# Performance work log

Measured on AMD Instinct MI355X. Metric: run time of the kernel, lower is better.

Reference implementation:

```python
import jax, jax.numpy as jnp
import numpy as np

GRID = 7          # grid_unit
NSAMPLE = 48      # sample_num
RADIUS = 0.3      # radiu_grid
FEAT = 128


def square_distance(src, dst):
    # src [B,N,C], dst [B,M,C] -> [B,N,M]
    d = -2.0 * jnp.einsum('bnc,bmc->bnm', src, dst)
    d = d + jnp.sum(src * src, -1)[:, :, None]
    d = d + jnp.sum(dst * dst, -1)[:, None, :]
    return d


def batch_norm(x):
    n = jnp.sqrt(jnp.sum(x * x, axis=2, keepdims=True) + 1e-8)
    return x / (n + 1e-10)


def query_ball_point(radius, nsample, xyz, new_xyz):
    B, N, _ = xyz.shape
    sqr = square_distance(new_xyz, xyz)                       # [B,S,N]
    gidx = jnp.where(sqr > radius ** 2, N, jnp.arange(N)[None, None, :])
    gidx = jnp.sort(gidx, axis=-1)[:, :, :nsample]            # [B,S,ns]
    first = gidx[:, :, :1]
    return jnp.where(gidx == N, first, gidx)


def index_points(points, idx):
    # points [B,N,C], idx [B,S,K] -> [B,S,K,C]
    return jax.vmap(lambda p, i: p[i])(points, idx)


def _forward(xyz, pts_feat, W0, b0, W1, b1, W_unet, index):
    B = xyz.shape[0]
    pts = jnp.transpose(xyz[:, 0:3, :], (0, 2, 1))            # [B,N,3]
    N = pts.shape[1]
    g = GRID

    # mlp0 / mlp1 (Conv1d(128,3,1)) + batch_norm
    oris = batch_norm(pts_feat @ W0.T + b0)                   # [B,N,3]
    nors = batch_norm(pts_feat @ W1.T + b1)                   # [B,N,3]

    # ---- rot_pts_3D ----
    gidx = query_ball_point(RADIUS, NSAMPLE, pts, pts)        # [B,N,48]
    group_pts = index_points(pts, gidx)                       # [B,N,48,3]
    group_feat = index_points(pts_feat, gidx).reshape(-1, NSAMPLE, FEAT)  # [BN,48,128]

    ori_rot90 = batch_norm(jnp.cross(oris, nors))
    ori_0 = batch_norm(jnp.cross(ori_rot90, nors))
    rot = jnp.concatenate([ori_0, ori_rot90, nors], axis=-1).reshape(-1, 3, 3)
    rot = jnp.transpose(rot, (0, 2, 1))                       # [BN,3,3]

    local = (group_pts - pts[:, :, None, :]).reshape(-1, NSAMPLE, 3)
    local_pts = jnp.einsum('bsc,bcd->bsd', local, rot)        # [BN,48,3]

    coords = jnp.round((local_pts + RADIUS) / (2 * RADIUS) * (g - 1)).astype(jnp.int32)
    coords = jnp.clip(coords, 0, g - 1)
    # faithful to the original flattening: x*g + y*g + z
    idx = coords[..., 0] * g + coords[..., 1] * g + coords[..., 2]  # [BN,48]

    BN = local_pts.shape[0]
    grid0 = jnp.zeros((BN, g * g * g, FEAT), dtype=pts_feat.dtype)
    feat3d = grid0.at[jnp.arange(BN)[:, None], idx].set(group_feat)  # [BN,343,128]

    # ---- UNet3D stand-in: [BN,128,7,7,7] -> [BN,3,7,7] via (channel,depth) projection
    feat5d = feat3d.reshape(BN, g, g, g, FEAT)
    feat_off = jnp.einsum('bijkc,ckd->bijd', feat5d, W_unet).reshape(BN, g * g, 3)

    # ---- rot_offset ----
    vals = jnp.array([[i * 0.01, j * 0.01, 0.0]
                      for i in range(-30, 36, 10)
                      for j in range(-30, 36, 10)], dtype=pts.dtype)   # [49,3]
    up = vals[None] + feat_off                                # [BN,49,3]
    pts_repeat = pts.reshape(-1, 1, 3)                        # [BN,1,3]
    pts_up = jnp.einsum('bsc,bdc->bsd', up, rot) + pts_repeat  # v @ rot^T

    pts_offset = pts_up[:, 24, :].reshape(B, -1, 3)           # [B,N,3]
    pts_ups = pts_up[:, index, :].reshape(B, -1, 3)           # [B,16N,3]
    return (oris, nors, pts_ups, pts_offset, pts_up)


def setup_inputs() -> dict:
    key = jax.random.key(0)
    ks = jax.random.split(key, 6)
    B, N, C = 2, 1024, 128
    xyz = jax.random.normal(ks[0], (B, 3, N), dtype=jnp.float32)
    pts_feat = jax.random.normal(ks[1], (B, N, C), dtype=jnp.float32)
    W0 = jax.random.normal(ks[2], (3, C), dtype=jnp.float32) * 0.05
    b0 = jnp.zeros((3,), dtype=jnp.float32)
    W1 = jax.random.normal(ks[3], (3, C), dtype=jnp.float32) * 0.05
    b1 = jnp.zeros((3,), dtype=jnp.float32)
    W_unet = jax.random.normal(ks[4], (C, GRID, 3), dtype=jnp.float32) * 0.02
    index = jax.random.randint(ks[5], (16,), 0, GRID * GRID)
    return {"xyz": xyz, "pts_feat": pts_feat, "W0": W0, "b0": b0,
            "W1": W1, "b1": b1, "W_unet": W_unet, "index": index}


def reference(xyz, pts_feat, W0, b0, W1, b1, W_unet, index):
    return _forward(xyz, pts_feat, W0, b0, W1, b1, W_unet, index)
```

## Files before the change

kernel.cpp:

```cpp
#include <hip/hip_runtime.h>

#define NB 2
#define NP 1024
#define NC 128
#define NG 7
#define NSM 48
#define BN (NB*NP)

#define OFF_ORIS 0
#define OFF_NORS (BN*3)
#define OFF_PUPS (2*BN*3)
#define OFF_POFF (OFF_PUPS + BN*16*3)
#define OFF_PU   (OFF_POFF + BN*3)

__device__ __forceinline__ void bnorm3(float v[3]) {
    float ss = __fadd_rn(__fadd_rn(__fmul_rn(v[0],v[0]), __fmul_rn(v[1],v[1])), __fmul_rn(v[2],v[2]));
    float nr = sqrtf(__fadd_rn(ss, 1e-8f));
    float dn = __fadd_rn(nr, 1e-10f);
    v[0] = __fdiv_rn(v[0], dn);
    v[1] = __fdiv_rn(v[1], dn);
    v[2] = __fdiv_rn(v[2], dn);
}

__global__ __launch_bounds__(64) void k1(const float* __restrict__ xyz,
                                         const float* __restrict__ feat,
                                         const float* __restrict__ W0, const float* __restrict__ b0,
                                         const float* __restrict__ W1, const float* __restrict__ b1,
                                         float* __restrict__ out,
                                         float* __restrict__ pts_ws,
                                         float* __restrict__ nrm_ws,
                                         float* __restrict__ rot_ws) {
    int p = blockIdx.x;
    int b = p >> 10, n = p & (NP - 1);
    int l = threadIdx.x;

    float f0 = feat[p*NC + l];
    float f1 = feat[p*NC + 64 + l];
    float s0 = f0*W0[l]     + f1*W0[64+l];
    float s1 = f0*W0[128+l] + f1*W0[192+l];
    float s2 = f0*W0[256+l] + f1*W0[320+l];
    float s3 = f0*W1[l]     + f1*W1[64+l];
    float s4 = f0*W1[128+l] + f1*W1[192+l];
    float s5 = f0*W1[256+l] + f1*W1[320+l];
    for (int off = 32; off; off >>= 1) {
        s0 += __shfl_xor(s0, off);
        s1 += __shfl_xor(s1, off);
        s2 += __shfl_xor(s2, off);
        s3 += __shfl_xor(s3, off);
        s4 += __shfl_xor(s4, off);
        s5 += __shfl_xor(s5, off);
    }
    if (l == 0) {
        float o[3]  = { s0 + b0[0], s1 + b0[1], s2 + b0[2] };
        float nn[3] = { s3 + b1[0], s4 + b1[1], s5 + b1[2] };
        bnorm3(o);
        bnorm3(nn);
        float r90[3];
        r90[0] = __fsub_rn(__fmul_rn(o[1], nn[2]), __fmul_rn(o[2], nn[1]));
        r90[1] = __fsub_rn(__fmul_rn(o[2], nn[0]), __fmul_rn(o[0], nn[2]));
        r90[2] = __fsub_rn(__fmul_rn(o[0], nn[1]), __fmul_rn(o[1], nn[0]));
        bnorm3(r90);
        float o0[3];
        o0[0] = __fsub_rn(__fmul_rn(r90[1], nn[2]), __fmul_rn(r90[2], nn[1]));
        o0[1] = __fsub_rn(__fmul_rn(r90[2], nn[0]), __fmul_rn(r90[0], nn[2]));
        o0[2] = __fsub_rn(__fmul_rn(r90[0], nn[1]), __fmul_rn(r90[1], nn[0]));
        bnorm3(o0);

        out[OFF_ORIS + p*3+0] = o[0];  out[OFF_ORIS + p*3+1] = o[1];  out[OFF_ORIS + p*3+2] = o[2];
        out[OFF_NORS + p*3+0] = nn[0]; out[OFF_NORS + p*3+1] = nn[1]; out[OFF_NORS + p*3+2] = nn[2];

        rot_ws[p*9+0] = o0[0];  rot_ws[p*9+1] = o0[1];  rot_ws[p*9+2] = o0[2];
        rot_ws[p*9+3] = r90[0]; rot_ws[p*9+4] = r90[1]; rot_ws[p*9+5] = r90[2];
        rot_ws[p*9+6] = nn[0];  rot_ws[p*9+7] = nn[1];  rot_ws[p*9+8] = nn[2];

        float px = xyz[(b*3+0)*NP + n];
        float py = xyz[(b*3+1)*NP + n];
        float pz = xyz[(b*3+2)*NP + n];
        pts_ws[p*3+0] = px; pts_ws[p*3+1] = py; pts_ws[p*3+2] = pz;
        nrm_ws[p] = __fadd_rn(__fadd_rn(__fmul_rn(px,px), __fmul_rn(py,py)), __fmul_rn(pz,pz));
    }
}

__global__ __launch_bounds__(256) void k2(const float* __restrict__ feat,
                                          const float* __restrict__ W_unet,
                                          const int* __restrict__ index,
                                          const float* __restrict__ pts_ws,
                                          const float* __restrict__ nrm_ws,
                                          const float* __restrict__ rot_ws,
                                          float* __restrict__ out) {
    __shared__ float spts[NP*3];
    __shared__ float snrm[NP];
    __shared__ float srot[9];
    __shared__ int   sgidx[NSM];
    __shared__ int   sidx[NSM];
    __shared__ int   swin[NSM];
    __shared__ float sfo[NG*NG*3];
    __shared__ float spu[NG*NG*3];

    int p = blockIdx.x;
    int b = p >> 10, n = p & (NP - 1);
    int tid = threadIdx.x;

    for (int i = tid; i < NP*3; i += 256) spts[i] = pts_ws[b*NP*3 + i];
    for (int i = tid; i < NP; i += 256)   snrm[i] = nrm_ws[b*NP + i];
    if (tid < 9) srot[tid] = rot_ws[p*9 + tid];
    if (tid < NG*NG*3) sfo[tid] = 0.0f;
    __syncthreads();

    if (tid < 64) {
        float cx = spts[n*3+0], cy = spts[n*3+1], cz = spts[n*3+2];
        float cn = snrm[n];
        int count = 0, first = -1;
        for (int base = 0; base < NP && count < NSM; base += 64) {
            int m = base + tid;
            float dot = __fadd_rn(__fadd_rn(__fmul_rn(cx, spts[m*3+0]),
                                            __fmul_rn(cy, spts[m*3+1])),
                                  __fmul_rn(cz, spts[m*3+2]));
            float d = __fadd_rn(__fadd_rn(__fmul_rn(-2.0f, dot), cn), snrm[m]);
            bool sel = !(d > 0.09f);
            unsigned long long mk = __ballot(sel);
            if (first < 0 && mk != 0ull) first = base + (__ffsll(mk) - 1);
            if (sel) {
                int pos = count + (int)__popcll(mk & ((1ull << tid) - 1ull));
                if (pos < NSM) sgidx[pos] = m;
            }
            count += (int)__popcll(mk);
        }
        if (first < 0) first = n;
        if (count < NSM) {
            for (int i = count + tid; i < NSM; i += 64) sgidx[i] = first;
        }
    }
    __syncthreads();

    if (tid < NSM) {
        int m = sgidx[tid];
        float lx = spts[m*3+0] - spts[n*3+0];
        float ly = spts[m*3+1] - spts[n*3+1];
        float lz = spts[m*3+2] - spts[n*3+2];
        int c[3];
        #pragma unroll
        for (int dd = 0; dd < 3; ++dd) {
            float lp = __fadd_rn(__fadd_rn(__fmul_rn(lx, srot[dd*3+0]),
                                           __fmul_rn(ly, srot[dd*3+1])),
                                 __fmul_rn(lz, srot[dd*3+2]));
            float t = rintf(__fmul_rn(__fdiv_rn(__fadd_rn(lp, 0.3f), 0.6f), 6.0f));
            int ci = (int)t;
            ci = ci < 0 ? 0 : (ci > 6 ? 6 : ci);
            c[dd] = ci;
        }
        sidx[tid] = c[0]*NG + c[1]*NG + c[2];
    }
    __syncthreads();

    if (tid < NSM) {
        int w = 1, my = sidx[tid];
        for (int s2 = tid + 1; s2 < NSM; ++s2)
            if (sidx[s2] == my) { w = 0; break; }
        swin[tid] = w;
    }
    __syncthreads();

    {
        int wid = tid >> 6, lane = tid & 63;
        for (int s = wid; s < NSM; s += 4) {
            if (!swin[s]) continue;
            int cell = sidx[s];
            int k = cell % NG;
            int q = cell / NG;
            int m = sgidx[s];
            const float* fr = feat + (size_t)(b*NP + m) * NC;
            float p0 = 0.f, p1 = 0.f, p2 = 0.f;
            #pragma unroll
            for (int cc = lane; cc < NC; cc += 64) {
                float f = fr[cc];
                const float* w = W_unet + cc*(NG*3) + k*3;
                p0 += f * w[0];
                p1 += f * w[1];
                p2 += f * w[2];
            }
            for (int off = 32; off; off >>= 1) {
                p0 += __shfl_xor(p0, off);
                p1 += __shfl_xor(p1, off);
                p2 += __shfl_xor(p2, off);
            }
            if (lane == 0) {
                atomicAdd(&sfo[q*3+0], p0);
                atomicAdd(&sfo[q*3+1], p1);
                atomicAdd(&sfo[q*3+2], p2);
            }
        }
    }
    __syncthreads();

    if (tid < NG*NG*3) {
        int q = tid / 3, d = tid % 3;
        int qi = q / NG, qj = q % NG;
        float v0 = (float)((-30 + 10*qi) * 0.01);
        float v1 = (float)((-30 + 10*qj) * 0.01);
        float u0 = __fadd_rn(v0, sfo[q*3+0]);
        float u1 = __fadd_rn(v1, sfo[q*3+1]);
        float u2 = sfo[q*3+2];
        float r = __fadd_rn(
                    __fadd_rn(
                      __fadd_rn(__fmul_rn(u0, srot[0*3+d]), __fmul_rn(u1, srot[1*3+d])),
                      __fmul_rn(u2, srot[2*3+d])),
                    spts[n*3+d]);
        spu[tid] = r;
        out[OFF_PU + p*(NG*NG*3) + tid] = r;
        if (q == 24) out[OFF_POFF + p*3 + d] = r;
    }
    __syncthreads();

    if (tid < 16*3) {
        int t = tid / 3, d = tid % 3;
        int q = index[t];
        out[OFF_PUPS + (p*16 + t)*3 + d] = spu[q*3 + d];
    }
}

extern "C" void kernel_launch(void* const* d_in, const int* in_sizes, int n_in,
                              void* d_out, int out_size, void* d_ws, size_t ws_size,
                              hipStream_t stream) {
    const float* xyz    = (const float*)d_in[0];
    const float* feat   = (const float*)d_in[1];
    const float* W0     = (const float*)d_in[2];
    const float* b0     = (const float*)d_in[3];
    const float* W1     = (const float*)d_in[4];
    const float* b1     = (const float*)d_in[5];
    const float* W_unet = (const float*)d_in[6];
    const int*   index  = (const int*)d_in[7];
    float* out = (float*)d_out;
    float* ws  = (float*)d_ws;

    float* pts_ws = ws;
    float* nrm_ws = ws + BN*3;
    float* rot_ws = ws + BN*3 + BN;

    hipLaunchKernelGGL(k1, dim3(BN), dim3(64), 0, stream,
                       xyz, feat, W0, b0, W1, b1, out, pts_ws, nrm_ws, rot_ws);
    hipLaunchKernelGGL(k2, dim3(BN), dim3(256), 0, stream,
                       feat, W_unet, index, pts_ws, nrm_ws, rot_ws, out);
}
```

Baseline: 89.08 us.

## Fuse projection and grouping kernels; parallelize ball query across all waves

Merges the per-point projection/rotation kernel into the grouping kernel, computing rotation into shared memory and loading xyz directly instead of round-tripping through workspace. The ball query now evaluates all 1024 candidates across four waves with ballot masks and a prefix-based compaction rather than a sequential early-exit scan in one wave. The feature gather is regrouped so 16-lane groups handle each sample with shorter reductions. Trades early exit and workspace reuse for more parallel work per block and one fewer launch.

New measurement: 78.80 us. 1.13x faster.

```diff
diff --git a/kernel.cpp b/kernel.cpp
--- a/kernel.cpp
+++ b/kernel.cpp
@@ -22,114 +22,122 @@
     v[2] = __fdiv_rn(v[2], dn);
 }
 
-__global__ __launch_bounds__(64) void k1(const float* __restrict__ xyz,
-                                         const float* __restrict__ feat,
-                                         const float* __restrict__ W0, const float* __restrict__ b0,
-                                         const float* __restrict__ W1, const float* __restrict__ b1,
-                                         float* __restrict__ out,
-                                         float* __restrict__ pts_ws,
-                                         float* __restrict__ nrm_ws,
-                                         float* __restrict__ rot_ws) {
-    int p = blockIdx.x;
-    int b = p >> 10, n = p & (NP - 1);
-    int l = threadIdx.x;
-
-    float f0 = feat[p*NC + l];
-    float f1 = feat[p*NC + 64 + l];
-    float s0 = f0*W0[l]     + f1*W0[64+l];
-    float s1 = f0*W0[128+l] + f1*W0[192+l];
-    float s2 = f0*W0[256+l] + f1*W0[320+l];
-    float s3 = f0*W1[l]     + f1*W1[64+l];
-    float s4 = f0*W1[128+l] + f1*W1[192+l];
-    float s5 = f0*W1[256+l] + f1*W1[320+l];
-    for (int off = 32; off; off >>= 1) {
-        s0 += __shfl_xor(s0, off);
-        s1 += __shfl_xor(s1, off);
-        s2 += __shfl_xor(s2, off);
-        s3 += __shfl_xor(s3, off);
-        s4 += __shfl_xor(s4, off);
-        s5 += __shfl_xor(s5, off);
-    }
-    if (l == 0) {
-        float o[3]  = { s0 + b0[0], s1 + b0[1], s2 + b0[2] };
-        float nn[3] = { s3 + b1[0], s4 + b1[1], s5 + b1[2] };
-        bnorm3(o);
-        bnorm3(nn);
-        float r90[3];
-        r90[0] = __fsub_rn(__fmul_rn(o[1], nn[2]), __fmul_rn(o[2], nn[1]));
-        r90[1] = __fsub_rn(__fmul_rn(o[2], nn[0]), __fmul_rn(o[0], nn[2]));
-        r90[2] = __fsub_rn(__fmul_rn(o[0], nn[1]), __fmul_rn(o[1], nn[0]));
-        bnorm3(r90);
-        float o0[3];
-        o0[0] = __fsub_rn(__fmul_rn(r90[1], nn[2]), __fmul_rn(r90[2], nn[1]));
-        o0[1] = __fsub_rn(__fmul_rn(r90[2], nn[0]), __fmul_rn(r90[0], nn[2]));
-        o0[2] = __fsub_rn(__fmul_rn(r90[0], nn[1]), __fmul_rn(r90[1], nn[0]));
-        bnorm3(o0);
-
-        out[OFF_ORIS + p*3+0] = o[0];  out[OFF_ORIS + p*3+1] = o[1];  out[OFF_ORIS + p*3+2] = o[2];
-        out[OFF_NORS + p*3+0] = nn[0]; out[OFF_NORS + p*3+1] = nn[1]; out[OFF_NORS + p*3+2] = nn[2];
-
-        rot_ws[p*9+0] = o0[0];  rot_ws[p*9+1] = o0[1];  rot_ws[p*9+2] = o0[2];
-        rot_ws[p*9+3] = r90[0]; rot_ws[p*9+4] = r90[1]; rot_ws[p*9+5] = r90[2];
-        rot_ws[p*9+6] = nn[0];  rot_ws[p*9+7] = nn[1];  rot_ws[p*9+8] = nn[2];
-
-        float px = xyz[(b*3+0)*NP + n];
-        float py = xyz[(b*3+1)*NP + n];
-        float pz = xyz[(b*3+2)*NP + n];
-        pts_ws[p*3+0] = px; pts_ws[p*3+1] = py; pts_ws[p*3+2] = pz;
-        nrm_ws[p] = __fadd_rn(__fadd_rn(__fmul_rn(px,px), __fmul_rn(py,py)), __fmul_rn(pz,pz));
-    }
-}
-
-__global__ __launch_bounds__(256) void k2(const float* __restrict__ feat,
-                                          const float* __restrict__ W_unet,
-                                          const int* __restrict__ index,
-                                          const float* __restrict__ pts_ws,
-                                          const float* __restrict__ nrm_ws,
-                                          const float* __restrict__ rot_ws,
-                                          float* __restrict__ out) {
+__global__ __launch_bounds__(256) void kfused(const float* __restrict__ xyz,
+                                              const float* __restrict__ feat,
+                                              const float* __restrict__ W0, const float* __restrict__ b0,
+                                              const float* __restrict__ W1, const float* __restrict__ b1,
+                                              const float* __restrict__ W_unet,
+                                              const int* __restrict__ index,
+                                              float* __restrict__ out) {
     __shared__ float spts[NP*3];
     __shared__ float snrm[NP];
     __shared__ float srot[9];
+    __shared__ unsigned long long smask[16];
     __shared__ int   sgidx[NSM];
     __shared__ int   sidx[NSM];
     __shared__ int   swin[NSM];
+    __shared__ int   scnt;
     __shared__ float sfo[NG*NG*3];
     __shared__ float spu[NG*NG*3];
 
     int p = blockIdx.x;
     int b = p >> 10, n = p & (NP - 1);
     int tid = threadIdx.x;
-
-    for (int i = tid; i < NP*3; i += 256) spts[i] = pts_ws[b*NP*3 + i];
-    for (int i = tid; i < NP; i += 256)   snrm[i] = nrm_ws[b*NP + i];
-    if (tid < 9) srot[tid] = rot_ws[p*9 + tid];
+    int w = tid >> 6, l = tid & 63;
+
     if (tid < NG*NG*3) sfo[tid] = 0.0f;
-    __syncthreads();
-
-    if (tid < 64) {
+
+    if (w == 0) {
+        float f0 = feat[p*NC + l];
+        float f1 = feat[p*NC + 64 + l];
+        float s0 = f0*W0[l]     + f1*W0[64+l];
+        float s1 = f0*W0[128+l] + f1*W0[192+l];
+        float s2 = f0*W0[256+l] + f1*W0[320+l];
+        float s3 = f0*W1[l]     + f1*W1[64+l];
+        float s4 = f0*W1[128+l] + f1*W1[192+l];
+        float s5 = f0*W1[256+l] + f1*W1[320+l];
+        for (int off = 32; off; off >>= 1) {
+            s0 += __shfl_xor(s0, off);
+            s1 += __shfl_xor(s1, off);
+            s2 += __shfl_xor(s2, off);
+            s3 += __shfl_xor(s3, off);
+            s4 += __shfl_xor(s4, off);
+            s5 += __shfl_xor(s5, off);
+        }
+        if (l == 0) {
+            float o[3]  = { s0 + b0[0], s1 + b0[1], s2 + b0[2] };
+            float nn[3] = { s3 + b1[0], s4 + b1[1], s5 + b1[2] };
+            bnorm3(o);
+            bnorm3(nn);
+            float r90[3];
+            r90[0] = __fsub_rn(__fmul_rn(o[1], nn[2]), __fmul_rn(o[2], nn[1]));
+            r90[1] = __fsub_rn(__fmul_rn(o[2], nn[0]), __fmul_rn(o[0], nn[2]));
+            r90[2] = __fsub_rn(__fmul_rn(o[0], nn[1]), __fmul_rn(o[1], nn[0]));
+            bnorm3(r90);
+            float o0[3];
+            o0[0] = __fsub_rn(__fmul_rn(r90[1], nn[2]), __fmul_rn(r90[2], nn[1]));
+            o0[1] = __fsub_rn(__fmul_rn(r90[2], nn[0]), __fmul_rn(r90[0], nn[2]));
+            o0[2] = __fsub_rn(__fmul_rn(r90[0], nn[1]), __fmul_rn(r90[1], nn[0]));
+            bnorm3(o0);
+
+            out[OFF_ORIS + p*3+0] = o[0];  out[OFF_ORIS + p*3+1] = o[1];  out[OFF_ORIS + p*3+2] = o[2];
+            out[OFF_NORS + p*3+0] = nn[0]; out[OFF_NORS + p*3+1] = nn[1]; out[OFF_NORS + p*3+2] = nn[2];
+
+            srot[0] = o0[0];  srot[1] = o0[1];  srot[2] = o0[2];
+            srot[3] = r90[0]; srot[4] = r90[1]; srot[5] = r90[2];
+            srot[6] = nn[0];  srot[7] = nn[1];  srot[8] = nn[2];
+        }
+    } else {
+        const float* xb = xyz + (size_t)b*3*NP;
+        for (int j = tid - 64; j < NP; j += 192) {
+            float px = xb[j];
+            float py = xb[NP + j];
+            float pz = xb[2*NP + j];
+            spts[j*3+0] = px; spts[j*3+1] = py; spts[j*3+2] = pz;
+            snrm[j] = __fadd_rn(__fadd_rn(__fmul_rn(px,px), __fmul_rn(py,py)), __fmul_rn(pz,pz));
+        }
+    }
+    __syncthreads();
+
+    {
         float cx = spts[n*3+0], cy = spts[n*3+1], cz = spts[n*3+2];
         float cn = snrm[n];
-        int count = 0, first = -1;
-        for (int base = 0; base < NP && count < NSM; base += 64) {
-            int m = base + tid;
+        #pragma unroll
+        for (int k = 0; k < 4; ++k) {
+            int m = ((w<<2) + k)*64 + l;
             float dot = __fadd_rn(__fadd_rn(__fmul_rn(cx, spts[m*3+0]),
                                             __fmul_rn(cy, spts[m*3+1])),
                                   __fmul_rn(cz, spts[m*3+2]));
             float d = __fadd_rn(__fadd_rn(__fmul_rn(-2.0f, dot), cn), snrm[m]);
             bool sel = !(d > 0.09f);
             unsigned long long mk = __ballot(sel);
-            if (first < 0 && mk != 0ull) first = base + (__ffsll(mk) - 1);
-            if (sel) {
-                int pos = count + (int)__popcll(mk & ((1ull << tid) - 1ull));
-                if (pos < NSM) sgidx[pos] = m;
-            }
-            count += (int)__popcll(mk);
-        }
-        if (first < 0) first = n;
-        if (count < NSM) {
-            for (int i = count + tid; i < NSM; i += 64) sgidx[i] = first;
-        }
+            if (l == 0) smask[(w<<2) + k] = mk;
+        }
+    }
+    __syncthreads();
+
+    if (tid < 16) {
+        unsigned long long wv = smask[tid];
+        int prefix = 0, total = 0;
+        #pragma unroll
+        for (int j = 0; j < 16; ++j) {
+            int pc = __popcll(smask[j]);
+            if (j < tid) prefix += pc;
+            total += pc;
+        }
+        if (tid == 0) scnt = total;
+        int pos = prefix;
+        while (wv && pos < NSM) {
+            int bpos = __ffsll(wv) - 1;
+            sgidx[pos++] = (tid << 6) + bpos;
+            wv &= wv - 1;
+        }
+    }
+    __syncthreads();
+
+    {
+        int total = scnt;
+        if (tid < NSM && tid >= total) sgidx[tid] = sgidx[0];
     }
     __syncthreads();
 
@@ -154,37 +162,44 @@
     __syncthreads();
 
     if (tid < NSM) {
-        int w = 1, my = sidx[tid];
+        int win = 1, my = sidx[tid];
         for (int s2 = tid + 1; s2 < NSM; ++s2)
-            if (sidx[s2] == my) { w = 0; break; }
-        swin[tid] = w;
+            if (sidx[s2] == my) { win = 0; break; }
+        swin[tid] = win;
     }
     __syncthreads();
 
     {
-        int wid = tid >> 6, lane = tid & 63;
-        for (int s = wid; s < NSM; s += 4) {
-            if (!swin[s]) continue;
-            int cell = sidx[s];
-            int k = cell % NG;
-            int q = cell / NG;
-            int m = sgidx[s];
-            const float* fr = feat + (size_t)(b*NP + m) * NC;
+        int sl = tid & 15;
+        int sg = tid >> 4;
+        #pragma unroll
+        for (int r = 0; r < 3; ++r) {
+            int s = r*16 + sg;
+            int act = swin[s];
+            int q = 0, k = 0;
             float p0 = 0.f, p1 = 0.f, p2 = 0.f;
+            if (act) {
+                int cell = sidx[s];
+                k = cell % NG;
+                q = cell / NG;
+                const float* fr = feat + (size_t)(b*NP + sgidx[s]) * NC;
+                #pragma unroll
+                for (int c8 = 0; c8 < 8; ++c8) {
+                    int cc = sl + c8*16;
+                    float f = fr[cc];
+                    const float* wp = W_unet + cc*(NG*3) + k*3;
+                    p0 += f * wp[0];
+                    p1 += f * wp[1];
+                    p2 += f * wp[2];
+                }
+            }
             #pragma unroll
-            for (int cc = lane; cc < NC; cc += 64) {
-                float f = fr[cc];
-                const float* w = W_unet + cc*(NG*3) + k*3;
-                p0 += f * w[0];
-                p1 += f * w[1];
-                p2 += f * w[2];
-            }
-            for (int off = 32; off; off >>= 1) {
+            for (int off = 8; off; off >>= 1) {
                 p0 += __shfl_xor(p0, off);
                 p1 += __shfl_xor(p1, off);
                 p2 += __shfl_xor(p2, off);
             }
-            if (lane == 0) {
+            if (act && sl == 0) {
                 atomicAdd(&sfo[q*3+0], p0);
                 atomicAdd(&sfo[q*3+1], p1);
                 atomicAdd(&sfo[q*3+2], p2);
@@ -231,14 +246,7 @@
     const float* W_unet = (const float*)d_in[6];
     const int*   index  = (const int*)d_in[7];
     float* out = (float*)d_out;
-    float* ws  = (float*)d_ws;
-
-    float* pts_ws = ws;
-    float* nrm_ws = ws + BN*3;
-    float* rot_ws = ws + BN*3 + BN;
-
-    hipLaunchKernelGGL(k1, dim3(BN), dim3(64), 0, stream,
-                       xyz, feat, W0, b0, W1, b1, out, pts_ws, nrm_ws, rot_ws);
-    hipLaunchKernelGGL(k2, dim3(BN), dim3(256), 0, stream,
-                       feat, W_unet, index, pts_ws, nrm_ws, rot_ws, out);
+
+    hipLaunchKernelGGL(kfused, dim3(BN), dim3(256), 0, stream,
+                       xyz, feat, W0, b0, W1, b1, W_unet, index, out);
 }
```
